# Kernel tuning notes

Measured on AMD Instinct MI355X. Metric: run time of the kernel, lower is better.

Reference implementation:

```python
import jax, jax.numpy as jnp
from jax import lax
import numpy as np

TEMPERATURE = 0.8
TOP_K = 50
TOP_P = 0.9
REP_PENALTY = 1.2


def setup_inputs() -> dict:
    key = jax.random.key(0)
    k1, k2 = jax.random.split(key)
    B, V, T = 256, 50257, 2048
    logits = jax.random.normal(k1, (B, V), dtype=jnp.float32) * 4.0  # spread so top-p is non-trivial
    generated = jax.random.randint(k2, (B, T), 0, V, dtype=jnp.int64)
    return {"logits": logits, "generated": generated}


def reference(logits, generated):
    """One decode-step of LLM.generate: temperature -> repetition penalty ->
    top-k filter -> top-p (nucleus) filter -> softmax -> multinomial sample.
    Returns (next_token [B], probs [B, V])."""
    B, V = logits.shape
    x = logits / TEMPERATURE

    # repetition penalty: divide logits at every previously-generated token id
    rows = jnp.arange(B)[:, None]
    present = jnp.zeros((B, V), dtype=bool).at[rows, generated].set(True)
    x = jnp.where(present, x / REP_PENALTY, x)

    # top-k: mask everything strictly below the k-th largest logit
    kth = lax.top_k(x, TOP_K)[0][:, -1:]  # [B, 1]
    x = jnp.where(x < kth, -jnp.inf, x)

    # top-p: sort descending, softmax, cumsum, drop tail mass > p (always keep top-1)
    order = jnp.argsort(-x, axis=-1)                      # [B, V] descending order
    sorted_logits = jnp.take_along_axis(x, order, axis=-1)
    cum = jnp.cumsum(jax.nn.softmax(sorted_logits, axis=-1), axis=-1)
    remove_sorted = (cum > TOP_P).at[:, 0].set(False)
    inv = jnp.argsort(order, axis=-1)                     # inverse permutation
    remove = jnp.take_along_axis(remove_sorted, inv, axis=-1)
    x = jnp.where(remove, -jnp.inf, x)

    probs = jax.nn.softmax(x, axis=-1)
    # multinomial sampling == categorical over the filtered logits
    next_token = jax.random.categorical(jax.random.key(42), x, axis=-1)  # [B]
    return next_token, probs
```

## Files before the change

### kernel.cpp

```cpp
#include <hip/hip_runtime.h>
#include <stdint.h>

#define V_CONST 50257
#define NMASK ((V_CONST + 31) / 32)
#define KTOP 50
#define CAND_CAP 1024
#define NTHREADS 1024
#define THR_SCREEN 13.0f
#define C_TEMP 1.25f
#define C_PEN ((float)(1.25 / 1.2))
#define THREEFRY_PARTITIONABLE 1

__device__ __forceinline__ void tf_round(uint32_t &x0, uint32_t &x1, int r) {
  x0 += x1;
  x1 = (x1 << r) | (x1 >> (32 - r));
  x1 ^= x0;
}

__device__ __forceinline__ uint2 threefry_k_0_42(uint32_t x0, uint32_t x1) {
  const uint32_t ks0 = 0u;
  const uint32_t ks1 = 42u;
  const uint32_t ks2 = 0x1BD11BDAu ^ 0u ^ 42u;
  x0 += ks0; x1 += ks1;
  tf_round(x0, x1, 13); tf_round(x0, x1, 15); tf_round(x0, x1, 26); tf_round(x0, x1, 6);
  x0 += ks1; x1 += ks2 + 1u;
  tf_round(x0, x1, 17); tf_round(x0, x1, 29); tf_round(x0, x1, 16); tf_round(x0, x1, 24);
  x0 += ks2; x1 += ks0 + 2u;
  tf_round(x0, x1, 13); tf_round(x0, x1, 15); tf_round(x0, x1, 26); tf_round(x0, x1, 6);
  x0 += ks0; x1 += ks1 + 3u;
  tf_round(x0, x1, 17); tf_round(x0, x1, 29); tf_round(x0, x1, 16); tf_round(x0, x1, 24);
  x0 += ks1; x1 += ks2 + 4u;
  tf_round(x0, x1, 13); tf_round(x0, x1, 15); tf_round(x0, x1, 26); tf_round(x0, x1, 6);
  x0 += ks2; x1 += ks0 + 5u;
  uint2 r; r.x = x0; r.y = x1; return r;
}

__device__ __forceinline__ float gumbel_at(uint32_t p, uint32_t half_total) {
  uint32_t bits;
#if THREEFRY_PARTITIONABLE
  uint2 o = threefry_k_0_42(0u, p);
  bits = o.x ^ o.y;
#else
  if (p < half_total) {
    uint2 o = threefry_k_0_42(p, p + half_total);
    bits = o.x;
  } else {
    uint2 o = threefry_k_0_42(p - half_total, p);
    bits = o.y;
  }
#endif
  uint32_t ub = (bits >> 9) | 0x3F800000u;
  float u = __uint_as_float(ub) - 1.0f;
  u = u + 1.17549435e-38f;
  u = fmaxf(1.17549435e-38f, u);
  return -logf(-logf(u));
}

__device__ __forceinline__ uint32_t f2u_desc(float f) {
  uint32_t b = __float_as_uint(f);
  return (b & 0x80000000u) ? ~b : (b | 0x80000000u);
}
__device__ __forceinline__ float u2f(uint32_t u) {
  uint32_t b = (u & 0x80000000u) ? (u & 0x7FFFFFFFu) : ~u;
  return __uint_as_float(b);
}

__global__ __launch_bounds__(NTHREADS) void sample_kernel(
    const float* __restrict__ logits, const int* __restrict__ generated,
    float* __restrict__ out, int B, int T) {
  const int b = blockIdx.x;
  const int tid = threadIdx.x;

  __shared__ uint32_t mask[NMASK];
  __shared__ uint32_t cu[CAND_CAP];
  __shared__ int      cidx[CAND_CAP];
  __shared__ uint32_t su[CAND_CAP];
  __shared__ int      sidx[CAND_CAP];
  __shared__ float    eg[CAND_CAP];
  __shared__ float    gg[CAND_CAP];
  __shared__ int s_ncand, s_nsurv, s_rlast;
  __shared__ float s_z2;

  for (int i = tid; i < NMASK; i += NTHREADS) mask[i] = 0u;
  if (tid == 0) s_ncand = 0;
  __syncthreads();
  const int* grow = generated + (size_t)b * T;
  for (int i = tid; i < T; i += NTHREADS) {
    int tok = grow[i];
    atomicOr(&mask[tok >> 5], 1u << (tok & 31));
  }
  __syncthreads();

  const float* lrow = logits + (size_t)b * V_CONST;
  float* prow = out + B + (size_t)b * V_CONST;
  const int aoff = (4 - (b & 3)) & 3;
  const int tailn = (V_CONST - aoff) & 3;
  const int body4 = (V_CONST - aoff) >> 2;
  const float4* arow4 = (const float4*)(lrow + aoff);
  float4* orow4 = (float4*)(prow + aoff);
  const float4 z4 = make_float4(0.f, 0.f, 0.f, 0.f);

#define SCREEN1(xv, vv) do {                                          \
    int v_ = (vv); float x_ = (xv);                                   \
    uint32_t pres_ = (mask[v_ >> 5] >> (v_ & 31)) & 1u;               \
    float m_ = pres_ ? C_PEN : C_TEMP;                                \
    if (x_ * m_ >= THR_SCREEN) {                                      \
      float xe_ = x_ / 0.8f; if (pres_) xe_ = xe_ / 1.2f;             \
      int p_ = atomicAdd(&s_ncand, 1);                                \
      if (p_ < CAND_CAP) { cu[p_] = f2u_desc(xe_); cidx[p_] = v_; }   \
    } } while (0)

  for (int t = tid; t < body4; t += NTHREADS) {
    float4 r = arow4[t];
    orow4[t] = z4;
    int v0 = aoff + (t << 2);
    SCREEN1(r.x, v0 + 0);
    SCREEN1(r.y, v0 + 1);
    SCREEN1(r.z, v0 + 2);
    SCREEN1(r.w, v0 + 3);
  }
  if (tid < aoff + tailn) {
    int v = (tid < aoff) ? tid : (V_CONST - tailn) + (tid - aoff);
    prow[v] = 0.f;
    SCREEN1(lrow[v], v);
  }
#undef SCREEN1
  __syncthreads();

  const int total = s_ncand;
  int n = (total < CAND_CAP) ? total : CAND_CAP;
  bool ok = false;

  if (total >= KTOP && total <= CAND_CAP) {
    for (int i = tid; i < n; i += NTHREADS) {
      uint32_t ui = cu[i]; int ii = cidx[i];
      int rank = 0;
      for (int j = 0; j < n; j++) {
        uint32_t uj = cu[j];
        rank += ((uj > ui) || (uj == ui && cidx[j] < ii)) ? 1 : 0;
      }
      su[rank] = ui; sidx[rank] = ii;
    }
    __syncthreads();
    ok = (su[KTOP - 1] >= f2u_desc(THR_SCREEN) + 64u);
  } else {
    __syncthreads();
  }

  if (!ok) {
    float thr = THR_SCREEN;
    uint32_t ulo_ = 0u, uhi_ = 0xFFFFFFFFu;
    n = 0;
    for (int attempt = 0; attempt < 64; ++attempt) {
      __syncthreads();
      if (tid == 0) s_ncand = 0;
      __syncthreads();
      for (int t = tid; t < body4; t += NTHREADS) {
        float4 r = arow4[t];
        int v0 = aoff + (t << 2);
        uint32_t w = (mask[v0 >> 5] >> (v0 & 31)) & 0xFu;
        float m0 = (w & 1u) ? C_PEN : C_TEMP;
        float m1 = (w & 2u) ? C_PEN : C_TEMP;
        float m2 = (w & 4u) ? C_PEN : C_TEMP;
        float m3 = (w & 8u) ? C_PEN : C_TEMP;
        if (r.x * m0 >= thr) { int p = atomicAdd(&s_ncand, 1); if (p < CAND_CAP) { cu[p] = __float_as_uint(r.x); cidx[p] = v0; } }
        if (r.y * m1 >= thr) { int p = atomicAdd(&s_ncand, 1); if (p < CAND_CAP) { cu[p] = __float_as_uint(r.y); cidx[p] = v0 + 1; } }
        if (r.z * m2 >= thr) { int p = atomicAdd(&s_ncand, 1); if (p < CAND_CAP) { cu[p] = __float_as_uint(r.z); cidx[p] = v0 + 2; } }
        if (r.w * m3 >= thr) { int p = atomicAdd(&s_ncand, 1); if (p < CAND_CAP) { cu[p] = __float_as_uint(r.w); cidx[p] = v0 + 3; } }
      }
      if (tid < aoff + tailn) {
        int v = (tid < aoff) ? tid : (V_CONST - tailn) + (tid - aoff);
        float x = lrow[v];
        float m = ((mask[v >> 5] >> (v & 31)) & 1u) ? C_PEN : C_TEMP;
        if (x * m >= thr) { int p = atomicAdd(&s_ncand, 1); if (p < CAND_CAP) { cu[p] = __float_as_uint(x); cidx[p] = v; } }
      }
      __syncthreads();
      const int tot = s_ncand;
      n = (tot < CAND_CAP) ? tot : CAND_CAP;
      const bool window = (tot >= KTOP && tot <= CAND_CAP);
      const bool last = (attempt == 63);
      if (window || last) {
        if (n > 0) {
          for (int i = tid; i < n; i += NTHREADS) {
            float x = __uint_as_float(cu[i]);
            int v = cidx[i];
            float xe = x / 0.8f;
            if ((mask[v >> 5] >> (v & 31)) & 1u) xe = xe / 1.2f;
            cu[i] = f2u_desc(xe);
          }
          __syncthreads();
          for (int i = tid; i < n; i += NTHREADS) {
            uint32_t ui = cu[i]; int ii = cidx[i];
            int rank = 0;
            for (int j = 0; j < n; j++) {
              uint32_t uj = cu[j];
              rank += ((uj > ui) || (uj == ui && cidx[j] < ii)) ? 1 : 0;
            }
            su[rank] = ui; sidx[rank] = ii;
          }
          __syncthreads();
        }
        if (window) {
          if (su[KTOP - 1] >= f2u_desc(thr) + 64u) break;
          if (last) break;
          thr = u2f(su[KTOP - 1] >= 96u ? su[KTOP - 1] - 96u : 0u);
        } else break;
      } else if (tot < KTOP) {
        uhi_ = f2u_desc(thr);
        if (attempt == 0) thr = 11.0f;
        else {
          uint32_t mid = ulo_ + (uhi_ - ulo_) / 2u;
          if (mid >= uhi_) mid = uhi_ - 1u;
          thr = u2f(mid);
        }
      } else {
        ulo_ = f2u_desc(thr);
        uint32_t mid = ulo_ + (uhi_ - ulo_) / 2u;
        if (mid <= ulo_) mid = ulo_ + 1u;
        thr = u2f(mid);
      }
    }
  }

  if (n == 0) { if (tid == 0) out[b] = 0.f; return; }

  if (tid == 0) {
    int kpos = (n < KTOP) ? (n - 1) : (KTOP - 1);
    uint32_t kth = su[kpos];
    int ns = kpos + 1;
    while (ns < n && su[ns] == kth) ns++;
    s_nsurv = ns;
  }
  __syncthreads();
  const int nsurv = s_nsurv;
  const float s0 = u2f(su[0]);
  const uint32_t half_total = (uint32_t)((size_t)256 * V_CONST / 2);

  for (int r = tid; r < nsurv; r += NTHREADS) {
    float f = u2f(su[r]);
    eg[r] = expf(f - s0);
    gg[r] = gumbel_at((uint32_t)(b * V_CONST + sidx[r]), half_total);
  }
  __syncthreads();

  if (tid == 0) {
    float zall = 0.f;
    for (int r = 0; r < nsurv; r++) zall += eg[r];
    float cum = 0.f;
    int rlast = 0;
    for (int r = 0; r < nsurv; r++) {
      cum += eg[r] / zall;
      if (r == 0 || cum <= 0.9f) rlast = r;
      else break;
    }
    float z2 = 0.f;
    for (int r = 0; r <= rlast; r++) z2 += eg[r];
    float best = -3.402823466e38f; int besti = V_CONST;
    for (int r = 0; r <= rlast; r++) {
      float sc = u2f(su[r]) + gg[r];
      int idx = sidx[r];
      if (sc > best || (sc == best && idx < besti)) { best = sc; besti = idx; }
    }
    out[b] = (float)besti;
    s_rlast = rlast; s_z2 = z2;
  }
  __syncthreads();
  const int rlast = s_rlast;
  const float z2 = s_z2;

  for (int r = tid; r <= rlast; r += NTHREADS) {
    prow[sidx[r]] = eg[r] / z2;
  }
}

extern "C" void kernel_launch(void* const* d_in, const int* in_sizes, int n_in,
                              void* d_out, int out_size, void* d_ws, size_t ws_size,
                              hipStream_t stream) {
  const float* logits = (const float*)d_in[0];
  const int* generated = (const int*)d_in[1];
  float* out = (float*)d_out;
  const int B = in_sizes[0] / V_CONST;
  const int T = in_sizes[1] / B;
  hipLaunchKernelGGL(sample_kernel, dim3(B), dim3(NTHREADS), 0, stream,
                     logits, generated, out, B, T);
}
```

Measured before the change: 32.76 us.

## Overlap mask build with logit screening and run sampling tail in one wavefront

The first screen now ignores the repetition mask. It uses the temperature-only multiplier, which is the larger one, so it still gives a superset of candidates, and it defers penalty application until after the mask is built. Token loads are issued before the logit scan, and the mask atomics run afterwards, removing one barrier and letting the global loads overlap. The scan is software-pipelined by prefetching the next float4. The serial thread-0 survivor count, softmax, top-p and argmax tail is replaced with a single 64-lane wavefront using shuffles and ballot, with the old path kept as a fallback when ties overflow 64.

```diff
diff --git a/kernel.cpp b/kernel.cpp
--- a/kernel.cpp
+++ b/kernel.cpp
@@ -78,18 +78,17 @@
   __shared__ int      sidx[CAND_CAP];
   __shared__ float    eg[CAND_CAP];
   __shared__ float    gg[CAND_CAP];
-  __shared__ int s_ncand, s_nsurv, s_rlast;
+  __shared__ int s_cnt, s_nsurv, s_ovf, s_rlast;
   __shared__ float s_z2;
 
   for (int i = tid; i < NMASK; i += NTHREADS) mask[i] = 0u;
-  if (tid == 0) s_ncand = 0;
+  if (tid == 0) s_cnt = 0;
   __syncthreads();
+
   const int* grow = generated + (size_t)b * T;
-  for (int i = tid; i < T; i += NTHREADS) {
-    int tok = grow[i];
-    atomicOr(&mask[tok >> 5], 1u << (tok & 31));
-  }
-  __syncthreads();
+  int toks[4];
+  int ntok = 0;
+  for (int i = tid; i < T && ntok < 4; i += NTHREADS) toks[ntok++] = grow[i];
 
   const float* lrow = logits + (size_t)b * V_CONST;
   float* prow = out + B + (size_t)b * V_CONST;
@@ -100,38 +99,61 @@
   float4* orow4 = (float4*)(prow + aoff);
   const float4 z4 = make_float4(0.f, 0.f, 0.f, 0.f);
 
-#define SCREEN1(xv, vv) do {                                          \
-    int v_ = (vv); float x_ = (xv);                                   \
-    uint32_t pres_ = (mask[v_ >> 5] >> (v_ & 31)) & 1u;               \
-    float m_ = pres_ ? C_PEN : C_TEMP;                                \
-    if (x_ * m_ >= THR_SCREEN) {                                      \
-      float xe_ = x_ / 0.8f; if (pres_) xe_ = xe_ / 1.2f;             \
-      int p_ = atomicAdd(&s_ncand, 1);                                \
-      if (p_ < CAND_CAP) { cu[p_] = f2u_desc(xe_); cidx[p_] = v_; }   \
-    } } while (0)
-
-  for (int t = tid; t < body4; t += NTHREADS) {
-    float4 r = arow4[t];
-    orow4[t] = z4;
-    int v0 = aoff + (t << 2);
-    SCREEN1(r.x, v0 + 0);
-    SCREEN1(r.y, v0 + 1);
-    SCREEN1(r.z, v0 + 2);
-    SCREEN1(r.w, v0 + 3);
-  }
-  if (tid < aoff + tailn) {
-    int v = (tid < aoff) ? tid : (V_CONST - tailn) + (tid - aoff);
-    prow[v] = 0.f;
-    SCREEN1(lrow[v], v);
-  }
-#undef SCREEN1
+#define PUSH_RAW(xv, vv) do {                                          \
+    int p_ = atomicAdd(&s_cnt, 1);                                     \
+    if (p_ < CAND_CAP) { cu[p_] = __float_as_uint(xv); cidx[p_] = (vv); } \
+  } while (0)
+
+  {
+    int t = tid;
+    bool has = (t < body4);
+    float4 rc;
+    if (has) rc = arow4[t];
+    while (has) {
+      int t2 = t + NTHREADS;
+      bool has2 = (t2 < body4);
+      float4 rn;
+      if (has2) rn = arow4[t2];
+      orow4[t] = z4;
+      int v0 = aoff + (t << 2);
+      if (rc.x * C_TEMP >= THR_SCREEN) PUSH_RAW(rc.x, v0 + 0);
+      if (rc.y * C_TEMP >= THR_SCREEN) PUSH_RAW(rc.y, v0 + 1);
+      if (rc.z * C_TEMP >= THR_SCREEN) PUSH_RAW(rc.z, v0 + 2);
+      if (rc.w * C_TEMP >= THR_SCREEN) PUSH_RAW(rc.w, v0 + 3);
+      t = t2; rc = rn; has = has2;
+    }
+    if (tid < aoff + tailn) {
+      int v = (tid < aoff) ? tid : (V_CONST - tailn) + (tid - aoff);
+      prow[v] = 0.f;
+      float x = lrow[v];
+      if (x * C_TEMP >= THR_SCREEN) PUSH_RAW(x, v);
+    }
+  }
+#undef PUSH_RAW
+
+  for (int k = 0; k < ntok; k++) {
+    int tok = toks[k];
+    atomicOr(&mask[tok >> 5], 1u << (tok & 31));
+  }
+  for (int i = tid + 4 * NTHREADS; i < T; i += NTHREADS) {
+    int tok = grow[i];
+    atomicOr(&mask[tok >> 5], 1u << (tok & 31));
+  }
   __syncthreads();
 
-  const int total = s_ncand;
+  const int total = s_cnt;
   int n = (total < CAND_CAP) ? total : CAND_CAP;
   bool ok = false;
 
   if (total >= KTOP && total <= CAND_CAP) {
+    for (int i = tid; i < n; i += NTHREADS) {
+      float x = __uint_as_float(cu[i]);
+      int v = cidx[i];
+      float xe = x / 0.8f;
+      if ((mask[v >> 5] >> (v & 31)) & 1u) xe = xe / 1.2f;
+      cu[i] = f2u_desc(xe);
+    }
+    __syncthreads();
     for (int i = tid; i < n; i += NTHREADS) {
       uint32_t ui = cu[i]; int ii = cidx[i];
       int rank = 0;
@@ -143,8 +165,6 @@
     }
     __syncthreads();
     ok = (su[KTOP - 1] >= f2u_desc(THR_SCREEN) + 64u);
-  } else {
-    __syncthreads();
   }
 
   if (!ok) {
@@ -153,7 +173,7 @@
     n = 0;
     for (int attempt = 0; attempt < 64; ++attempt) {
       __syncthreads();
-      if (tid == 0) s_ncand = 0;
+      if (tid == 0) s_cnt = 0;
       __syncthreads();
       for (int t = tid; t < body4; t += NTHREADS) {
         float4 r = arow4[t];
@@ -163,19 +183,19 @@
         float m1 = (w & 2u) ? C_PEN : C_TEMP;
         float m2 = (w & 4u) ? C_PEN : C_TEMP;
         float m3 = (w & 8u) ? C_PEN : C_TEMP;
-        if (r.x * m0 >= thr) { int p = atomicAdd(&s_ncand, 1); if (p < CAND_CAP) { cu[p] = __float_as_uint(r.x); cidx[p] = v0; } }
-        if (r.y * m1 >= thr) { int p = atomicAdd(&s_ncand, 1); if (p < CAND_CAP) { cu[p] = __float_as_uint(r.y); cidx[p] = v0 + 1; } }
-        if (r.z * m2 >= thr) { int p = atomicAdd(&s_ncand, 1); if (p < CAND_CAP) { cu[p] = __float_as_uint(r.z); cidx[p] = v0 + 2; } }
-        if (r.w * m3 >= thr) { int p = atomicAdd(&s_ncand, 1); if (p < CAND_CAP) { cu[p] = __float_as_uint(r.w); cidx[p] = v0 + 3; } }
+        if (r.x * m0 >= thr) { int p = atomicAdd(&s_cnt, 1); if (p < CAND_CAP) { cu[p] = __float_as_uint(r.x); cidx[p] = v0; } }
+        if (r.y * m1 >= thr) { int p = atomicAdd(&s_cnt, 1); if (p < CAND_CAP) { cu[p] = __float_as_uint(r.y); cidx[p] = v0 + 1; } }
+        if (r.z * m2 >= thr) { int p = atomicAdd(&s_cnt, 1); if (p < CAND_CAP) { cu[p] = __float_as_uint(r.z); cidx[p] = v0 + 2; } }
+        if (r.w * m3 >= thr) { int p = atomicAdd(&s_cnt, 1); if (p < CAND_CAP) { cu[p] = __float_as_uint(r.w); cidx[p] = v0 + 3; } }
       }
       if (tid < aoff + tailn) {
         int v = (tid < aoff) ? tid : (V_CONST - tailn) + (tid - aoff);
         float x = lrow[v];
         float m = ((mask[v >> 5] >> (v & 31)) & 1u) ? C_PEN : C_TEMP;
-        if (x * m >= thr) { int p = atomicAdd(&s_ncand, 1); if (p < CAND_CAP) { cu[p] = __float_as_uint(x); cidx[p] = v; } }
+        if (x * m >= thr) { int p = atomicAdd(&s_cnt, 1); if (p < CAND_CAP) { cu[p] = __float_as_uint(x); cidx[p] = v; } }
       }
       __syncthreads();
-      const int tot = s_ncand;
+      const int tot = s_cnt;
       n = (tot < CAND_CAP) ? tot : CAND_CAP;
       const bool window = (tot >= KTOP && tot <= CAND_CAP);
       const bool last = (attempt == 63);
@@ -224,52 +244,93 @@
 
   if (n == 0) { if (tid == 0) out[b] = 0.f; return; }
 
-  if (tid == 0) {
+  if (tid < 64) {
+    int n64 = (n < 64) ? n : 64;
+    uint32_t sur = (tid < n64) ? su[tid] : 0u;
     int kpos = (n < KTOP) ? (n - 1) : (KTOP - 1);
-    uint32_t kth = su[kpos];
-    int ns = kpos + 1;
-    while (ns < n && su[ns] == kth) ns++;
-    s_nsurv = ns;
+    uint32_t kth = __shfl(sur, kpos, 64);
+    unsigned long long m = __ballot(tid < n64 && sur == kth);
+    int hi = 63 - __clzll(m);
+    if (tid == 0) {
+      s_nsurv = hi + 1;
+      s_ovf = (hi == n64 - 1 && n > n64) ? 1 : 0;
+    }
   }
   __syncthreads();
-  const int nsurv = s_nsurv;
-  const float s0 = u2f(su[0]);
+
   const uint32_t half_total = (uint32_t)((size_t)256 * V_CONST / 2);
 
-  for (int r = tid; r < nsurv; r += NTHREADS) {
-    float f = u2f(su[r]);
-    eg[r] = expf(f - s0);
-    gg[r] = gumbel_at((uint32_t)(b * V_CONST + sidx[r]), half_total);
-  }
-  __syncthreads();
-
-  if (tid == 0) {
-    float zall = 0.f;
-    for (int r = 0; r < nsurv; r++) zall += eg[r];
-    float cum = 0.f;
-    int rlast = 0;
-    for (int r = 0; r < nsurv; r++) {
-      cum += eg[r] / zall;
-      if (r == 0 || cum <= 0.9f) rlast = r;
-      else break;
-    }
-    float z2 = 0.f;
-    for (int r = 0; r <= rlast; r++) z2 += eg[r];
-    float best = -3.402823466e38f; int besti = V_CONST;
-    for (int r = 0; r <= rlast; r++) {
-      float sc = u2f(su[r]) + gg[r];
-      int idx = sidx[r];
-      if (sc > best || (sc == best && idx < besti)) { best = sc; besti = idx; }
-    }
-    out[b] = (float)besti;
-    s_rlast = rlast; s_z2 = z2;
-  }
-  __syncthreads();
-  const int rlast = s_rlast;
-  const float z2 = s_z2;
-
-  for (int r = tid; r <= rlast; r += NTHREADS) {
-    prow[sidx[r]] = eg[r] / z2;
+  if (!s_ovf) {
+    if (tid < 64) {
+      const int nsurv = s_nsurv;
+      uint32_t sur = (tid < nsurv) ? su[tid] : 0u;
+      int sidr = (tid < nsurv) ? sidx[tid] : 0x7FFFFFFF;
+      float f = u2f(sur);
+      float s0 = __shfl(f, 0, 64);
+      float egr = 0.f, ggr = 0.f;
+      if (tid < nsurv) {
+        egr = expf(f - s0);
+        ggr = gumbel_at((uint32_t)(b * V_CONST + sidr), half_total);
+      }
+      float scr = f + ggr;
+      float zall = 0.f;
+      for (int j = 0; j < nsurv; j++) zall += __shfl(egr, j, 64);
+      float cum = 0.f, z2 = 0.f;
+      int rlast = 0;
+      float best = -3.402823466e38f; int besti = V_CONST;
+      for (int j = 0; j < nsurv; j++) {
+        float e = __shfl(egr, j, 64);
+        cum += e / zall;
+        if (j == 0 || cum <= 0.9f) {
+          rlast = j;
+          z2 += e;
+          float sc = __shfl(scr, j, 64);
+          int idx = __shfl(sidr, j, 64);
+          if (sc > best || (sc == best && idx < besti)) { best = sc; besti = idx; }
+        } else break;
+      }
+      if (tid == 0) out[b] = (float)besti;
+      if (tid <= rlast) prow[sidr] = egr / z2;
+    }
+    return;
+  }
+
+  {
+    const int nsurv = s_nsurv;
+    const float s0 = u2f(su[0]);
+    for (int r = tid; r < nsurv; r += NTHREADS) {
+      float f = u2f(su[r]);
+      eg[r] = expf(f - s0);
+      gg[r] = gumbel_at((uint32_t)(b * V_CONST + sidx[r]), half_total);
+    }
+    __syncthreads();
+    if (tid == 0) {
+      float zall = 0.f;
+      for (int r = 0; r < nsurv; r++) zall += eg[r];
+      float cum = 0.f;
+      int rlast = 0;
+      for (int r = 0; r < nsurv; r++) {
+        cum += eg[r] / zall;
+        if (r == 0 || cum <= 0.9f) rlast = r;
+        else break;
+      }
+      float z2 = 0.f;
+      for (int r = 0; r <= rlast; r++) z2 += eg[r];
+      float best = -3.402823466e38f; int besti = V_CONST;
+      for (int r = 0; r <= rlast; r++) {
+        float sc = u2f(su[r]) + gg[r];
+        int idx = sidx[r];
+        if (sc > best || (sc == best && idx < besti)) { best = sc; besti = idx; }
+      }
+      out[b] = (float)besti;
+      s_rlast = rlast; s_z2 = z2;
+    }
+    __syncthreads();
+    const int rlast = s_rlast;
+    const float z2 = s_z2;
+    for (int r = tid; r <= rlast; r += NTHREADS) {
+      prow[sidx[r]] = eg[r] / z2;
+    }
   }
 }
 
```

New measurement: 34.16 us. 1.04x slower.
